# Kernel optimization log

Measured on AMD Instinct MI355X. Metric: run time of the kernel, lower is better.

The kernel has to match this reference:

```python
import jax, jax.numpy as jnp
import numpy as np
from jax import lax

DIM = 256
NUM_HEADS = 8
HEAD_DIM = DIM // NUM_HEADS          # 32
KEY_DIM = int(HEAD_DIM * 0.5)        # 16
SCALE = KEY_DIM ** -0.5
H_QKV = DIM + KEY_DIM * NUM_HEADS * 2  # 512
BN_EPS = 1e-3  # keras BatchNormalization default epsilon


def conv_bn(x, w, gamma, beta, mean, var, groups=1):
    # Conv2D (no bias) + BatchNorm (inference), activation=None
    y = lax.conv_general_dilated(
        x, w, window_strides=(1, 1), padding='SAME',
        dimension_numbers=('NHWC', 'HWIO', 'NHWC'),
        feature_group_count=groups)
    return gamma * (y - mean) * lax.rsqrt(var + BN_EPS) + beta


def setup_inputs() -> dict:
    key = jax.random.key(0)
    ks = jax.random.split(key, 4)
    B, Hs, Ws = 8, 32, 32
    inp = {
        'inputs': jax.random.normal(ks[0], (B, Hs, Ws, DIM), dtype=jnp.float32),
        # qkv: 1x1 conv dim -> h
        'qkv_w': jax.random.normal(ks[1], (1, 1, DIM, H_QKV), dtype=jnp.float32) * 0.05,
        'qkv_gamma': jnp.ones((H_QKV,), jnp.float32),
        'qkv_beta': jnp.zeros((H_QKV,), jnp.float32),
        'qkv_mean': jnp.zeros((H_QKV,), jnp.float32),
        'qkv_var': jnp.ones((H_QKV,), jnp.float32),
        # pe: 3x3 depthwise conv (groups=dim)
        'pe_w': jax.random.normal(ks[2], (3, 3, 1, DIM), dtype=jnp.float32) * 0.05,
        'pe_gamma': jnp.ones((DIM,), jnp.float32),
        'pe_beta': jnp.zeros((DIM,), jnp.float32),
        'pe_mean': jnp.zeros((DIM,), jnp.float32),
        'pe_var': jnp.ones((DIM,), jnp.float32),
        # proj: 1x1 conv dim -> dim
        'proj_w': jax.random.normal(ks[3], (1, 1, DIM, DIM), dtype=jnp.float32) * 0.05,
        'proj_gamma': jnp.ones((DIM,), jnp.float32),
        'proj_beta': jnp.zeros((DIM,), jnp.float32),
        'proj_mean': jnp.zeros((DIM,), jnp.float32),
        'proj_var': jnp.ones((DIM,), jnp.float32),
    }
    return inp


def reference(inputs, qkv_w, qkv_gamma, qkv_beta, qkv_mean, qkv_var,
              pe_w, pe_gamma, pe_beta, pe_mean, pe_var,
              proj_w, proj_gamma, proj_beta, proj_mean, proj_var):
    B, Hs, Ws, C = inputs.shape
    N = Hs * Ws
    x = conv_bn(inputs, qkv_w, qkv_gamma, qkv_beta, qkv_mean, qkv_var)  # [B,H,W,h]
    x = x.reshape(B, N, NUM_HEADS, 2 * KEY_DIM + HEAD_DIM)
    q = x[..., :KEY_DIM]                          # [B,N,nh,kd]
    k = x[..., KEY_DIM:2 * KEY_DIM]               # [B,N,nh,kd]
    v = x[..., 2 * KEY_DIM:]                      # [B,N,nh,hd]
    # attn = q^T @ k^T : [B,nh,N,N]
    attn = jnp.einsum('bnhk,bmhk->bhnm', q, k) * SCALE
    attn = jax.nn.softmax(attn, axis=-1)
    # x = v^T @ attn : [B,nh,hd,N]
    x = jnp.einsum('bnhd,bhnm->bhdm', v, attn)
    # faithful to source: transpose [0,2,1,3] -> [B,hd,nh,N], then reshape NHWC
    x = jnp.transpose(x, (0, 2, 1, 3)).reshape(B, Hs, Ws, C)
    pe = conv_bn(v.reshape(B, Hs, Ws, C), pe_w, pe_gamma, pe_beta, pe_mean, pe_var, groups=C)
    x = x + pe
    x = conv_bn(x, proj_w, proj_gamma, proj_beta, proj_mean, proj_var)
    return x
```

## Files before the change

kernel.cpp:

```cpp
#include <hip/hip_runtime.h>

typedef _Float16 h4 __attribute__((ext_vector_type(4)));
typedef _Float16 h8 __attribute__((ext_vector_type(8)));
typedef float    f4 __attribute__((ext_vector_type(4)));

#define QSCALE (0.25f * 1.44269504088896f)

__device__ __forceinline__ float ex2(float x){ return __builtin_amdgcn_exp2f(x); }

__global__ __launch_bounds__(256) void prep_k(
    const float* __restrict__ qkvw, const float* __restrict__ qg, const float* __restrict__ qb,
    const float* __restrict__ qm,   const float* __restrict__ qv,
    const float* __restrict__ pew,  const float* __restrict__ pg, const float* __restrict__ pb,
    const float* __restrict__ pm,   const float* __restrict__ pv,
    const float* __restrict__ prw,  const float* __restrict__ prg, const float* __restrict__ prb,
    const float* __restrict__ prm,  const float* __restrict__ prv,
    _Float16* __restrict__ Wqkv, float* __restrict__ bqkv,
    _Float16* __restrict__ Wproj, float* __restrict__ bproj,
    float* __restrict__ peW, float* __restrict__ peB)
{
  const int gid = blockIdx.x*256 + threadIdx.x;
  const int gsz = gridDim.x*256;
  for (int i = gid; i < 512*256; i += gsz){
    int o = i >> 8, c = i & 255;
    float s = qg[o] * rsqrtf(qv[o] + 1e-3f);
    Wqkv[i] = (_Float16)(qkvw[c*512 + o] * s);
  }
  for (int i = gid; i < 512; i += gsz){
    float s = qg[i] * rsqrtf(qv[i] + 1e-3f);
    bqkv[i] = qb[i] - qm[i]*s;
  }
  for (int i = gid; i < 256*256; i += gsz){
    int o = i >> 8, c = i & 255;
    float s = prg[o] * rsqrtf(prv[o] + 1e-3f);
    Wproj[i] = (_Float16)(prw[c*256 + o] * s);
  }
  for (int i = gid; i < 256; i += gsz){
    float s = prg[i] * rsqrtf(prv[i] + 1e-3f);
    bproj[i] = prb[i] - prm[i]*s;
  }
  for (int i = gid; i < 9*256; i += gsz){
    int c = i & 255;
    float s = pg[c] * rsqrtf(pv[c] + 1e-3f);
    peW[i] = pew[i] * s;
  }
  for (int i = gid; i < 256; i += gsz){
    float s = pg[i] * rsqrtf(pv[i] + 1e-3f);
    peB[i] = pb[i] - pm[i]*s;
  }
}

__global__ __launch_bounds__(256) void qkv_gemm_k(
    const float* __restrict__ X, const _Float16* __restrict__ Wqkv,
    const float* __restrict__ bias,
    _Float16* __restrict__ Qh, _Float16* __restrict__ Kh, _Float16* __restrict__ Vh)
{
  __shared__ __align__(16) _Float16 As[64*136];
  __shared__ __align__(16) _Float16 Bs[64*136];
  const int t = threadIdx.x, lane = t & 63, wv = t >> 6;
  const int l15 = lane & 15, q = lane >> 4;
  const int wr = wv & 1, wc = wv >> 1;
  const int m0 = blockIdx.x*64, n0 = blockIdx.y*64;
  const int ar = t >> 2, ac = t & 3;
  float4 av[8]; uint4 bv[4];
  #pragma unroll
  for (int i = 0; i < 8; ++i){
    int idx = i*256 + t, row = idx >> 5, c4 = idx & 31;
    av[i] = *(const float4*)(X + (size_t)(m0+row)*256 + c4*4);
  }
  #pragma unroll
  for (int i = 0; i < 4; ++i){
    int idx = i*256 + t, row = idx >> 4, seg = idx & 15;
    bv[i] = *(const uint4*)(Wqkv + (size_t)(n0+row)*256 + seg*8);
  }
  f4 acc[2][2] = {};
  #pragma unroll
  for (int kc = 0; kc < 2; ++kc){
    #pragma unroll
    for (int i = 0; i < 8; ++i){
      int idx = i*256 + t, row = idx >> 5, c4 = idx & 31;
      h4 o; o[0]=(_Float16)av[i].x; o[1]=(_Float16)av[i].y;
            o[2]=(_Float16)av[i].z; o[3]=(_Float16)av[i].w;
      *(h4*)&As[row*136 + c4*4] = o;
    }
    #pragma unroll
    for (int i = 0; i < 4; ++i){
      int idx = i*256 + t, row = idx >> 4, seg = idx & 15;
      *(uint4*)&Bs[row*136 + seg*8] = bv[i];
    }
    __syncthreads();
    if (kc == 0){
      #pragma unroll
      for (int i = 0; i < 8; ++i){
        int idx = i*256 + t, row = idx >> 5, c4 = idx & 31;
        av[i] = *(const float4*)(X + (size_t)(m0+row)*256 + 128 + c4*4);
      }
      #pragma unroll
      for (int i = 0; i < 4; ++i){
        int idx = i*256 + t, row = idx >> 4, seg = idx & 15;
        bv[i] = *(const uint4*)(Wqkv + (size_t)(n0+row)*256 + 128 + seg*8);
      }
    }
    #pragma unroll
    for (int kk = 0; kk < 4; ++kk){
      h8 af[2], bf[2];
      #pragma unroll
      for (int mi = 0; mi < 2; ++mi)
        af[mi] = *(const h8*)&As[(wr*32 + mi*16 + l15)*136 + kk*32 + q*8];
      #pragma unroll
      for (int nj = 0; nj < 2; ++nj)
        bf[nj] = *(const h8*)&Bs[(wc*32 + nj*16 + l15)*136 + kk*32 + q*8];
      #pragma unroll
      for (int mi = 0; mi < 2; ++mi)
      #pragma unroll
      for (int nj = 0; nj < 2; ++nj)
        acc[mi][nj] = __builtin_amdgcn_mfma_f32_16x16x32_f16(af[mi], bf[nj], acc[mi][nj], 0,0,0);
    }
    __syncthreads();
  }
  #pragma unroll
  for (int mi = 0; mi < 2; ++mi)
  #pragma unroll
  for (int nj = 0; nj < 2; ++nj){
    const int og = n0 + wc*32 + nj*16 + l15;
    const int h = og >> 6, j = og & 63;
    const float bs = bias[og];
    #pragma unroll
    for (int r = 0; r < 4; ++r){
      const int mg = m0 + wr*32 + mi*16 + q*4 + r;
      const int b = mg >> 10, n = mg & 1023;
      const size_t bhn = (size_t)(b*8+h)*1024 + n;
      const float v = acc[mi][nj][r] + bs;
      if (j < 16)      Qh[bhn*16 + j]      = (_Float16)(v * QSCALE);
      else if (j < 32) Kh[bhn*16 + (j-16)] = (_Float16)v;
      else             Vh[bhn*32 + (j-32)] = (_Float16)v;
    }
  }
}

__global__ __launch_bounds__(256) void proj_gemm_k(
    const _Float16* __restrict__ A, const _Float16* __restrict__ Wproj,
    const float* __restrict__ bias, float* __restrict__ Out)
{
  __shared__ __align__(16) _Float16 As[64*136];
  __shared__ __align__(16) _Float16 Bs[64*136];
  const int t = threadIdx.x, lane = t & 63, wv = t >> 6;
  const int l15 = lane & 15, q = lane >> 4;
  const int wr = wv & 1, wc = wv >> 1;
  const int m0 = blockIdx.x*64, n0 = blockIdx.y*64;
  uint4 av[4], bv[4];
  #pragma unroll
  for (int i = 0; i < 4; ++i){
    int idx = i*256 + t, row = idx >> 4, seg = idx & 15;
    av[i] = *(const uint4*)(A     + (size_t)(m0+row)*256 + seg*8);
    bv[i] = *(const uint4*)(Wproj + (size_t)(n0+row)*256 + seg*8);
  }
  f4 acc[2][2] = {};
  #pragma unroll
  for (int kc = 0; kc < 2; ++kc){
    #pragma unroll
    for (int i = 0; i < 4; ++i){
      int idx = i*256 + t, row = idx >> 4, seg = idx & 15;
      *(uint4*)&As[row*136 + seg*8] = av[i];
      *(uint4*)&Bs[row*136 + seg*8] = bv[i];
    }
    __syncthreads();
    if (kc == 0){
      #pragma unroll
      for (int i = 0; i < 4; ++i){
        int idx = i*256 + t, row = idx >> 4, seg = idx & 15;
        av[i] = *(const uint4*)(A     + (size_t)(m0+row)*256 + 128 + seg*8);
        bv[i] = *(const uint4*)(Wproj + (size_t)(n0+row)*256 + 128 + seg*8);
      }
    }
    #pragma unroll
    for (int kk = 0; kk < 4; ++kk){
      h8 af[2], bf[2];
      #pragma unroll
      for (int mi = 0; mi < 2; ++mi)
        af[mi] = *(const h8*)&As[(wr*32 + mi*16 + l15)*136 + kk*32 + q*8];
      #pragma unroll
      for (int nj = 0; nj < 2; ++nj)
        bf[nj] = *(const h8*)&Bs[(wc*32 + nj*16 + l15)*136 + kk*32 + q*8];
      #pragma unroll
      for (int mi = 0; mi < 2; ++mi)
      #pragma unroll
      for (int nj = 0; nj < 2; ++nj)
        acc[mi][nj] = __builtin_amdgcn_mfma_f32_16x16x32_f16(af[mi], bf[nj], acc[mi][nj], 0,0,0);
    }
    __syncthreads();
  }
  #pragma unroll
  for (int mi = 0; mi < 2; ++mi)
  #pragma unroll
  for (int nj = 0; nj < 2; ++nj){
    const int og = n0 + wc*32 + nj*16 + l15;
    const float bs = bias[og];
    #pragma unroll
    for (int r = 0; r < 4; ++r){
      const int mg = m0 + wr*32 + mi*16 + q*4 + r;
      Out[(size_t)mg*256 + og] = acc[mi][nj][r] + bs;
    }
  }
}

__global__ __launch_bounds__(256) void pass1_k(
    const _Float16* __restrict__ Qh, const _Float16* __restrict__ Kh,
    const _Float16* __restrict__ Vh, _Float16* __restrict__ Vs)
{
  __shared__ __align__(16) _Float16 Ks[1024*20];
  const int t = threadIdx.x, lane = t & 63, wv = t >> 6;
  const int l15 = lane & 15, q = lane >> 4;
  const int bh = blockIdx.y;
  const int n0 = blockIdx.x*128 + wv*32;
  const size_t qb = (size_t)bh*1024;
  const _Float16* kp = Kh + qb*16;
  #pragma unroll
  for (int i = 0; i < 8; ++i){
    int idx = i*256 + t, row = idx >> 1, seg = idx & 1;
    *(uint4*)&Ks[row*20 + seg*8] = *(const uint4*)(kp + row*16 + seg*8);
  }
  const h4 af0 = *(const h4*)(Qh + (qb + n0 + l15)*16 + q*4);
  const h4 af1 = *(const h4*)(Qh + (qb + n0 + 16 + l15)*16 + q*4);
  __syncthreads();
  f4 sm0 = {0.f,0.f,0.f,0.f}, sm1 = {0.f,0.f,0.f,0.f};
  #pragma unroll 8
  for (int mt = 0; mt < 64; ++mt){
    h4 bf = *(const h4*)&Ks[(mt*16 + l15)*20 + q*4];
    f4 z = {0.f,0.f,0.f,0.f};
    f4 d0 = __builtin_amdgcn_mfma_f32_16x16x16f16(af0, bf, z, 0,0,0);
    f4 d1 = __builtin_amdgcn_mfma_f32_16x16x16f16(af1, bf, z, 0,0,0);
    #pragma unroll
    for (int r = 0; r < 4; ++r){ sm0[r] += ex2(d0[r]); sm1[r] += ex2(d1[r]); }
  }
  #pragma unroll
  for (int st = 1; st < 16; st <<= 1){
    #pragma unroll
    for (int r = 0; r < 4; ++r){
      sm0[r] += __shfl_xor(sm0[r], st, 64);
      sm1[r] += __shfl_xor(sm1[r], st, 64);
    }
  }
  f4 cv0, cv1;
  #pragma unroll
  for (int r = 0; r < 4; ++r){ cv0[r] = 1.0f/sm0[r]; cv1[r] = 1.0f/sm1[r]; }
  #pragma unroll
  for (int half = 0; half < 2; ++half){
    const int dd = l15 + half*16;
    h4 o0, o1;
    #pragma unroll
    for (int r = 0; r < 4; ++r){
      o0[r] = (_Float16)((float)Vh[(qb + n0 + q*4 + r)*32 + dd] * cv0[r]);
      o1[r] = (_Float16)((float)Vh[(qb + n0 + 16 + q*4 + r)*32 + dd] * cv1[r]);
    }
    *(h4*)(Vs + ((size_t)bh*32 + dd)*1024 + n0 + q*4)      = o0;
    *(h4*)(Vs + ((size_t)bh*32 + dd)*1024 + n0 + 16 + q*4) = o1;
  }
}

__global__ __launch_bounds__(256) void pass2_k(
    const _Float16* __restrict__ Qh, const _Float16* __restrict__ Kh,
    const _Float16* __restrict__ Vs, _Float16* __restrict__ X1h)
{
  __shared__ __align__(16) char smem[1024*20*2 + 32*264*2];
  _Float16* Qs  = (_Float16*)smem;
  _Float16* Vss = (_Float16*)(smem + 40960);
  float*    Tt  = (float*)smem;
  const int t = threadIdx.x, lane = t & 63, wv = t >> 6;
  const int l15 = lane & 15, q = lane >> 4;
  const int bh = blockIdx.y;
  const int b  = bh >> 3, h = bh & 7;
  const int mb = blockIdx.x*128 + wv*32;
  const size_t qb = (size_t)bh*1024;
  const h4 kf0 = *(const h4*)(Kh + (qb + mb + l15)*16 + q*4);
  const h4 kf1 = *(const h4*)(Kh + (qb + mb + 16 + l15)*16 + q*4);
  const _Float16* qp = Qh + qb*16;
  const _Float16* vp = Vs + (size_t)bh*32*1024;
  #pragma unroll
  for (int i = 0; i < 8; ++i){
    int idx = i*256 + t, row = idx >> 1, seg = idx & 1;
    *(uint4*)&Qs[row*20 + seg*8] = *(const uint4*)(qp + row*16 + seg*8);
  }
  uint4 vr[4];
  #pragma unroll
  for (int i = 0; i < 4; ++i){
    int idx = i*256 + t, d = idx >> 5, seg = idx & 31;
    vr[i] = *(const uint4*)(vp + (size_t)d*1024 + seg*8);
  }
  f4 a00={0.f,0.f,0.f,0.f}, a01={0.f,0.f,0.f,0.f};
  f4 a10={0.f,0.f,0.f,0.f}, a11={0.f,0.f,0.f,0.f};
  for (int c = 0; c < 4; ++c){
    const int nt = c*256;
    #pragma unroll
    for (int i = 0; i < 4; ++i){
      int idx = i*256 + t, d = idx >> 5, seg = idx & 31;
      *(uint4*)&Vss[d*264 + seg*8] = vr[i];
    }
    __syncthreads();
    if (c < 3){
      #pragma unroll
      for (int i = 0; i < 4; ++i){
        int idx = i*256 + t, d = idx >> 5, seg = idx & 31;
        vr[i] = *(const uint4*)(vp + (size_t)d*1024 + nt + 256 + seg*8);
      }
    }
    #pragma unroll 4
    for (int sub = 0; sub < 16; ++sub){
      h4 qf = *(const h4*)&Qs[(nt + sub*16 + l15)*20 + q*4];
      h4 b0 = *(const h4*)&Vss[l15*264      + sub*16 + q*4];
      h4 b1 = *(const h4*)&Vss[(16+l15)*264 + sub*16 + q*4];
      f4 z = {0.f,0.f,0.f,0.f};
      f4 s0 = __builtin_amdgcn_mfma_f32_16x16x16f16(qf, kf0, z, 0,0,0);
      f4 s1 = __builtin_amdgcn_mfma_f32_16x16x16f16(qf, kf1, z, 0,0,0);
      h4 p0, p1;
      #pragma unroll
      for (int r = 0; r < 4; ++r){ p0[r] = (_Float16)ex2(s0[r]); p1[r] = (_Float16)ex2(s1[r]); }
      a00 = __builtin_amdgcn_mfma_f32_16x16x16f16(p0, b0, a00, 0,0,0);
      a01 = __builtin_amdgcn_mfma_f32_16x16x16f16(p0, b1, a01, 0,0,0);
      a10 = __builtin_amdgcn_mfma_f32_16x16x16f16(p1, b0, a10, 0,0,0);
      a11 = __builtin_amdgcn_mfma_f32_16x16x16f16(p1, b1, a11, 0,0,0);
    }
    __syncthreads();
  }
  float* tw = Tt + wv*(32*33);
  #pragma unroll
  for (int r = 0; r < 4; ++r){
    tw[(q*4 + r)*33      + l15]      = a00[r];
    tw[(q*4 + r)*33      + 16 + l15] = a01[r];
    tw[(16 + q*4 + r)*33 + l15]      = a10[r];
    tw[(16 + q*4 + r)*33 + 16 + l15] = a11[r];
  }
  __syncthreads();
  _Float16* xb = X1h + (size_t)b*262144 + (size_t)h*1024 + mb;
  const int mloc = lane & 31, dh = lane >> 5;
  #pragma unroll
  for (int r = 0; r < 16; ++r){
    const int d = r*2 + dh;
    xb[(size_t)d*8192 + mloc] = (_Float16)tw[mloc*33 + d];
  }
}

__global__ __launch_bounds__(256) void pe_add_k(
    const _Float16* __restrict__ Vh, const _Float16* __restrict__ X1h,
    const float* __restrict__ peW, const float* __restrict__ peB,
    _Float16* __restrict__ X2h)
{
  const int u = blockIdx.x*256 + threadIdx.x;
  const int c0 = (u & 31) * 8;
  const int tok = u >> 5;
  const int b = tok >> 10, n = tok & 1023;
  const int hs = n >> 5, ws = n & 31;
  const int h = c0 >> 5, d0 = c0 & 31;
  const size_t idx8 = (size_t)tok*256 + c0;
  float acc[8];
  {
    f4 b0v = *(const f4*)(peB + c0), b1v = *(const f4*)(peB + c0 + 4);
    #pragma unroll
    for (int j = 0; j < 4; ++j){ acc[j] = b0v[j]; acc[4+j] = b1v[j]; }
  }
  const _Float16* vb = Vh + (size_t)(b*8 + h)*32768 + d0;
  #pragma unroll
  for (int dy = 0; dy < 3; ++dy){
    const int y = hs + dy - 1;
    if ((unsigned)y < 32u){
      #pragma unroll
      for (int dx = 0; dx < 3; ++dx){
        const int x = ws + dx - 1;
        if ((unsigned)x < 32u){
          const int kk = dy*3 + dx;
          h8 vv = *(const h8*)(vb + (size_t)(y*32 + x)*32);
          f4 w0 = *(const f4*)(peW + kk*256 + c0);
          f4 w1 = *(const f4*)(peW + kk*256 + c0 + 4);
          #pragma unroll
          for (int j = 0; j < 4; ++j){
            acc[j]   += w0[j] * (float)vv[j];
            acc[4+j] += w1[j] * (float)vv[4+j];
          }
        }
      }
    }
  }
  h8 x1 = *(const h8*)(X1h + idx8);
  h8 o;
  #pragma unroll
  for (int j = 0; j < 8; ++j) o[j] = (_Float16)((float)x1[j] + acc[j]);
  *(h8*)(X2h + idx8) = o;
}

extern "C" void kernel_launch(void* const* d_in, const int* in_sizes, int n_in,
                              void* d_out, int out_size, void* d_ws, size_t ws_size,
                              hipStream_t stream)
{
  const float* X    = (const float*)d_in[0];
  const float* qkvw = (const float*)d_in[1];
  const float* qg   = (const float*)d_in[2];
  const float* qb   = (const float*)d_in[3];
  const float* qm   = (const float*)d_in[4];
  const float* qv   = (const float*)d_in[5];
  const float* pew  = (const float*)d_in[6];
  const float* pg   = (const float*)d_in[7];
  const float* pb   = (const float*)d_in[8];
  const float* pm   = (const float*)d_in[9];
  const float* pv   = (const float*)d_in[10];
  const float* prw  = (const float*)d_in[11];
  const float* prg  = (const float*)d_in[12];
  const float* prb  = (const float*)d_in[13];
  const float* prm  = (const float*)d_in[14];
  const float* prv  = (const float*)d_in[15];

  char* ws = (char*)d_ws;
  _Float16* X2h   = (_Float16*)(ws + 0);
  _Float16* Qh    = (_Float16*)(ws + 4194304);
  _Float16* Kh    = (_Float16*)(ws + 6291456);
  _Float16* Vh    = (_Float16*)(ws + 8388608);
  _Float16* Vs    = (_Float16*)(ws + 12582912);
  _Float16* X1h   = (_Float16*)(ws + 16777216);
  _Float16* Wqkv  = (_Float16*)(ws + 20971520);
  float*    bqkv  = (float*)   (ws + 21233664);
  _Float16* Wproj = (_Float16*)(ws + 21235712);
  float*    bproj = (float*)   (ws + 21366784);
  float*    peW   = (float*)   (ws + 21367808);
  float*    peB   = (float*)   (ws + 21377024);

  prep_k<<<64, 256, 0, stream>>>(qkvw, qg, qb, qm, qv, pew, pg, pb, pm, pv,
                                 prw, prg, prb, prm, prv,
                                 Wqkv, bqkv, Wproj, bproj, peW, peB);
  qkv_gemm_k<<<dim3(128, 8), 256, 0, stream>>>(X, Wqkv, bqkv, Qh, Kh, Vh);
  pass1_k<<<dim3(8, 64), 256, 0, stream>>>(Qh, Kh, Vh, Vs);
  pass2_k<<<dim3(8, 64), 256, 0, stream>>>(Qh, Kh, Vs, X1h);
  pe_add_k<<<1024, 256, 0, stream>>>(Vh, X1h, peW, peB, X2h);
  proj_gemm_k<<<dim3(128, 4), 256, 0, stream>>>(X2h, Wproj, bproj, (float*)d_out);
}
```

Before: 185.7 us.

## Stream K/Q/V through small LDS tiles in attention passes to raise occupancy

Pass1 and pass2 used to load the whole 1024-row K (or Q) plus a 256-column V chunk into shared memory per block, about 40-57KB of LDS. They now stream 128-row chunks with register double-buffering, cutting LDS to about 6-17KB so more blocks can be resident per CU. The grid is also transposed so consecutive block IDs step through different batch-heads. The cost is eight barrier pairs per block instead of one or four, and less work between each sync.

```diff
diff --git a/kernel.cpp b/kernel.cpp
--- a/kernel.cpp
+++ b/kernel.cpp
@@ -61,7 +61,6 @@
   const int l15 = lane & 15, q = lane >> 4;
   const int wr = wv & 1, wc = wv >> 1;
   const int m0 = blockIdx.x*64, n0 = blockIdx.y*64;
-  const int ar = t >> 2, ac = t & 3;
   float4 av[8]; uint4 bv[4];
   #pragma unroll
   for (int i = 0; i < 8; ++i){
@@ -208,30 +207,32 @@
     const _Float16* __restrict__ Qh, const _Float16* __restrict__ Kh,
     const _Float16* __restrict__ Vh, _Float16* __restrict__ Vs)
 {
-  __shared__ __align__(16) _Float16 Ks[1024*20];
+  __shared__ __align__(16) _Float16 Ks[128*24];
   const int t = threadIdx.x, lane = t & 63, wv = t >> 6;
   const int l15 = lane & 15, q = lane >> 4;
-  const int bh = blockIdx.y;
-  const int n0 = blockIdx.x*128 + wv*32;
+  const int bh = blockIdx.x;
+  const int n0 = blockIdx.y*128 + wv*32;
   const size_t qb = (size_t)bh*1024;
-  const _Float16* kp = Kh + qb*16;
-  #pragma unroll
-  for (int i = 0; i < 8; ++i){
-    int idx = i*256 + t, row = idx >> 1, seg = idx & 1;
-    *(uint4*)&Ks[row*20 + seg*8] = *(const uint4*)(kp + row*16 + seg*8);
-  }
   const h4 af0 = *(const h4*)(Qh + (qb + n0 + l15)*16 + q*4);
   const h4 af1 = *(const h4*)(Qh + (qb + n0 + 16 + l15)*16 + q*4);
-  __syncthreads();
+  const _Float16* kp = Kh + qb*16;
+  const int row = t >> 1, seg = t & 1;
+  uint4 kr = *(const uint4*)(kp + row*16 + seg*8);
   f4 sm0 = {0.f,0.f,0.f,0.f}, sm1 = {0.f,0.f,0.f,0.f};
-  #pragma unroll 8
-  for (int mt = 0; mt < 64; ++mt){
-    h4 bf = *(const h4*)&Ks[(mt*16 + l15)*20 + q*4];
-    f4 z = {0.f,0.f,0.f,0.f};
-    f4 d0 = __builtin_amdgcn_mfma_f32_16x16x16f16(af0, bf, z, 0,0,0);
-    f4 d1 = __builtin_amdgcn_mfma_f32_16x16x16f16(af1, bf, z, 0,0,0);
-    #pragma unroll
-    for (int r = 0; r < 4; ++r){ sm0[r] += ex2(d0[r]); sm1[r] += ex2(d1[r]); }
+  for (int c = 0; c < 8; ++c){
+    *(uint4*)&Ks[row*24 + seg*8] = kr;
+    __syncthreads();
+    if (c < 7) kr = *(const uint4*)(kp + ((c+1)*128 + row)*16 + seg*8);
+    #pragma unroll
+    for (int sub = 0; sub < 8; ++sub){
+      h4 bf = *(const h4*)&Ks[(sub*16 + l15)*24 + q*4];
+      f4 z = {0.f,0.f,0.f,0.f};
+      f4 d0 = __builtin_amdgcn_mfma_f32_16x16x16f16(af0, bf, z, 0,0,0);
+      f4 d1 = __builtin_amdgcn_mfma_f32_16x16x16f16(af1, bf, z, 0,0,0);
+      #pragma unroll
+      for (int r = 0; r < 4; ++r){ sm0[r] += ex2(d0[r]); sm1[r] += ex2(d1[r]); }
+    }
+    __syncthreads();
   }
   #pragma unroll
   for (int st = 1; st < 16; st <<= 1){
@@ -262,53 +263,43 @@
     const _Float16* __restrict__ Qh, const _Float16* __restrict__ Kh,
     const _Float16* __restrict__ Vs, _Float16* __restrict__ X1h)
 {
-  __shared__ __align__(16) char smem[1024*20*2 + 32*264*2];
+  __shared__ __align__(16) char smem[16896];
   _Float16* Qs  = (_Float16*)smem;
-  _Float16* Vss = (_Float16*)(smem + 40960);
+  _Float16* Vss = (_Float16*)(smem + 6144);
   float*    Tt  = (float*)smem;
   const int t = threadIdx.x, lane = t & 63, wv = t >> 6;
   const int l15 = lane & 15, q = lane >> 4;
-  const int bh = blockIdx.y;
+  const int bh = blockIdx.x;
   const int b  = bh >> 3, h = bh & 7;
-  const int mb = blockIdx.x*128 + wv*32;
+  const int mb = blockIdx.y*128 + wv*32;
   const size_t qb = (size_t)bh*1024;
   const h4 kf0 = *(const h4*)(Kh + (qb + mb + l15)*16 + q*4);
   const h4 kf1 = *(const h4*)(Kh + (qb + mb + 16 + l15)*16 + q*4);
   const _Float16* qp = Qh + qb*16;
   const _Float16* vp = Vs + (size_t)bh*32*1024;
-  #pragma unroll
-  for (int i = 0; i < 8; ++i){
-    int idx = i*256 + t, row = idx >> 1, seg = idx & 1;
-    *(uint4*)&Qs[row*20 + seg*8] = *(const uint4*)(qp + row*16 + seg*8);
-  }
-  uint4 vr[4];
-  #pragma unroll
-  for (int i = 0; i < 4; ++i){
-    int idx = i*256 + t, d = idx >> 5, seg = idx & 31;
-    vr[i] = *(const uint4*)(vp + (size_t)d*1024 + seg*8);
-  }
+  const int row = t >> 1, seg = t & 1;
+  const int vd = t >> 4, vseg = t & 15;
+  uint4 qr = *(const uint4*)(qp + row*16 + seg*8);
+  uint4 vr0 = *(const uint4*)(vp + (size_t)vd*1024      + vseg*8);
+  uint4 vr1 = *(const uint4*)(vp + (size_t)(vd+16)*1024 + vseg*8);
   f4 a00={0.f,0.f,0.f,0.f}, a01={0.f,0.f,0.f,0.f};
   f4 a10={0.f,0.f,0.f,0.f}, a11={0.f,0.f,0.f,0.f};
-  for (int c = 0; c < 4; ++c){
-    const int nt = c*256;
-    #pragma unroll
-    for (int i = 0; i < 4; ++i){
-      int idx = i*256 + t, d = idx >> 5, seg = idx & 31;
-      *(uint4*)&Vss[d*264 + seg*8] = vr[i];
-    }
-    __syncthreads();
-    if (c < 3){
-      #pragma unroll
-      for (int i = 0; i < 4; ++i){
-        int idx = i*256 + t, d = idx >> 5, seg = idx & 31;
-        vr[i] = *(const uint4*)(vp + (size_t)d*1024 + nt + 256 + seg*8);
-      }
-    }
-    #pragma unroll 4
-    for (int sub = 0; sub < 16; ++sub){
-      h4 qf = *(const h4*)&Qs[(nt + sub*16 + l15)*20 + q*4];
-      h4 b0 = *(const h4*)&Vss[l15*264      + sub*16 + q*4];
-      h4 b1 = *(const h4*)&Vss[(16+l15)*264 + sub*16 + q*4];
+  for (int c = 0; c < 8; ++c){
+    *(uint4*)&Qs[row*24 + seg*8] = qr;
+    *(uint4*)&Vss[vd*136      + vseg*8] = vr0;
+    *(uint4*)&Vss[(vd+16)*136 + vseg*8] = vr1;
+    __syncthreads();
+    if (c < 7){
+      const int nn = (c+1)*128;
+      qr  = *(const uint4*)(qp + (nn + row)*16 + seg*8);
+      vr0 = *(const uint4*)(vp + (size_t)vd*1024      + nn + vseg*8);
+      vr1 = *(const uint4*)(vp + (size_t)(vd+16)*1024 + nn + vseg*8);
+    }
+    #pragma unroll
+    for (int sub = 0; sub < 8; ++sub){
+      h4 qf = *(const h4*)&Qs[(sub*16 + l15)*24 + q*4];
+      h4 b0 = *(const h4*)&Vss[l15*136      + sub*16 + q*4];
+      h4 b1 = *(const h4*)&Vss[(16+l15)*136 + sub*16 + q*4];
       f4 z = {0.f,0.f,0.f,0.f};
       f4 s0 = __builtin_amdgcn_mfma_f32_16x16x16f16(qf, kf0, z, 0,0,0);
       f4 s1 = __builtin_amdgcn_mfma_f32_16x16x16f16(qf, kf1, z, 0,0,0);
@@ -426,8 +417,8 @@
                                  prw, prg, prb, prm, prv,
                                  Wqkv, bqkv, Wproj, bproj, peW, peB);
   qkv_gemm_k<<<dim3(128, 8), 256, 0, stream>>>(X, Wqkv, bqkv, Qh, Kh, Vh);
-  pass1_k<<<dim3(8, 64), 256, 0, stream>>>(Qh, Kh, Vh, Vs);
-  pass2_k<<<dim3(8, 64), 256, 0, stream>>>(Qh, Kh, Vs, X1h);
+  pass1_k<<<dim3(64, 8), 256, 0, stream>>>(Qh, Kh, Vh, Vs);
+  pass2_k<<<dim3(64, 8), 256, 0, stream>>>(Qh, Kh, Vs, X1h);
   pe_add_k<<<1024, 256, 0, stream>>>(Vh, X1h, peW, peB, X2h);
   proj_gemm_k<<<dim3(128, 4), 256, 0, stream>>>(X2h, Wproj, bproj, (float*)d_out);
 }
```

Result: faster. 159.1 us (-14.4%).

## Split attention passes along the key dimension across wave pairs to double block count

Applied to the files above, without the earlier changes.

Both attention passes now give each block 64 query/key rows instead of 128 and split the 1024-long reduction dimension between two wave pairs. Partial softmax sums and partial PV accumulators are combined through shared memory. K and Q/V tiles are streamed in 128-row chunks with register prefetch rather than staged whole, which shrinks LDS use. The goal is twice as many blocks (1024 per pass on 256 CUs) and higher occupancy, at the cost of extra syncs and a shared-memory reduction.

```diff
diff --git a/kernel.cpp b/kernel.cpp
--- a/kernel.cpp
+++ b/kernel.cpp
@@ -61,7 +61,6 @@
   const int l15 = lane & 15, q = lane >> 4;
   const int wr = wv & 1, wc = wv >> 1;
   const int m0 = blockIdx.x*64, n0 = blockIdx.y*64;
-  const int ar = t >> 2, ac = t & 3;
   float4 av[8]; uint4 bv[4];
   #pragma unroll
   for (int i = 0; i < 8; ++i){
@@ -208,30 +207,49 @@
     const _Float16* __restrict__ Qh, const _Float16* __restrict__ Kh,
     const _Float16* __restrict__ Vh, _Float16* __restrict__ Vs)
 {
-  __shared__ __align__(16) _Float16 Ks[1024*20];
+  __shared__ __align__(16) _Float16 Ks[2][128*24];
+  __shared__ float red[2][2][32];
   const int t = threadIdx.x, lane = t & 63, wv = t >> 6;
   const int l15 = lane & 15, q = lane >> 4;
+  const int g = wv & 1, mh = wv >> 1;
   const int bh = blockIdx.y;
-  const int n0 = blockIdx.x*128 + wv*32;
+  const int n0 = blockIdx.x*64 + g*32;
   const size_t qb = (size_t)bh*1024;
-  const _Float16* kp = Kh + qb*16;
-  #pragma unroll
-  for (int i = 0; i < 8; ++i){
-    int idx = i*256 + t, row = idx >> 1, seg = idx & 1;
-    *(uint4*)&Ks[row*20 + seg*8] = *(const uint4*)(kp + row*16 + seg*8);
-  }
   const h4 af0 = *(const h4*)(Qh + (qb + n0 + l15)*16 + q*4);
   const h4 af1 = *(const h4*)(Qh + (qb + n0 + 16 + l15)*16 + q*4);
-  __syncthreads();
+  const _Float16* kp = Kh + qb*16;
+  const int tidp = g*64 + lane;
+  uint4 kr[2];
+  #pragma unroll
+  for (int i = 0; i < 2; ++i){
+    int idx = i*128 + tidp, row = idx >> 1, seg = idx & 1;
+    kr[i] = *(const uint4*)(kp + (mh*512 + row)*16 + seg*8);
+  }
   f4 sm0 = {0.f,0.f,0.f,0.f}, sm1 = {0.f,0.f,0.f,0.f};
-  #pragma unroll 8
-  for (int mt = 0; mt < 64; ++mt){
-    h4 bf = *(const h4*)&Ks[(mt*16 + l15)*20 + q*4];
-    f4 z = {0.f,0.f,0.f,0.f};
-    f4 d0 = __builtin_amdgcn_mfma_f32_16x16x16f16(af0, bf, z, 0,0,0);
-    f4 d1 = __builtin_amdgcn_mfma_f32_16x16x16f16(af1, bf, z, 0,0,0);
-    #pragma unroll
-    for (int r = 0; r < 4; ++r){ sm0[r] += ex2(d0[r]); sm1[r] += ex2(d1[r]); }
+  for (int c = 0; c < 4; ++c){
+    #pragma unroll
+    for (int i = 0; i < 2; ++i){
+      int idx = i*128 + tidp, row = idx >> 1, seg = idx & 1;
+      *(uint4*)&Ks[mh][row*24 + seg*8] = kr[i];
+    }
+    __syncthreads();
+    if (c < 3){
+      #pragma unroll
+      for (int i = 0; i < 2; ++i){
+        int idx = i*128 + tidp, row = idx >> 1, seg = idx & 1;
+        kr[i] = *(const uint4*)(kp + (mh*512 + (c+1)*128 + row)*16 + seg*8);
+      }
+    }
+    #pragma unroll
+    for (int sub = 0; sub < 8; ++sub){
+      h4 bf = *(const h4*)&Ks[mh][(sub*16 + l15)*24 + q*4];
+      f4 z = {0.f,0.f,0.f,0.f};
+      f4 d0 = __builtin_amdgcn_mfma_f32_16x16x16f16(af0, bf, z, 0,0,0);
+      f4 d1 = __builtin_amdgcn_mfma_f32_16x16x16f16(af1, bf, z, 0,0,0);
+      #pragma unroll
+      for (int r = 0; r < 4; ++r){ sm0[r] += ex2(d0[r]); sm1[r] += ex2(d1[r]); }
+    }
+    __syncthreads();
   }
   #pragma unroll
   for (int st = 1; st < 16; st <<= 1){
@@ -241,74 +259,93 @@
       sm1[r] += __shfl_xor(sm1[r], st, 64);
     }
   }
-  f4 cv0, cv1;
-  #pragma unroll
-  for (int r = 0; r < 4; ++r){ cv0[r] = 1.0f/sm0[r]; cv1[r] = 1.0f/sm1[r]; }
-  #pragma unroll
-  for (int half = 0; half < 2; ++half){
-    const int dd = l15 + half*16;
-    h4 o0, o1;
-    #pragma unroll
-    for (int r = 0; r < 4; ++r){
-      o0[r] = (_Float16)((float)Vh[(qb + n0 + q*4 + r)*32 + dd] * cv0[r]);
-      o1[r] = (_Float16)((float)Vh[(qb + n0 + 16 + q*4 + r)*32 + dd] * cv1[r]);
-    }
-    *(h4*)(Vs + ((size_t)bh*32 + dd)*1024 + n0 + q*4)      = o0;
-    *(h4*)(Vs + ((size_t)bh*32 + dd)*1024 + n0 + 16 + q*4) = o1;
-  }
+  if (l15 == 0){
+    #pragma unroll
+    for (int r = 0; r < 4; ++r){
+      red[g][mh][q*4 + r]      = sm0[r];
+      red[g][mh][16 + q*4 + r] = sm1[r];
+    }
+  }
+  __syncthreads();
+  const int dd = l15 + mh*16;
+  h4 o0, o1;
+  #pragma unroll
+  for (int r = 0; r < 4; ++r){
+    const float cv0 = 1.0f/(red[g][0][q*4 + r]      + red[g][1][q*4 + r]);
+    const float cv1 = 1.0f/(red[g][0][16 + q*4 + r] + red[g][1][16 + q*4 + r]);
+    o0[r] = (_Float16)((float)Vh[(qb + n0 + q*4 + r)*32 + dd] * cv0);
+    o1[r] = (_Float16)((float)Vh[(qb + n0 + 16 + q*4 + r)*32 + dd] * cv1);
+  }
+  *(h4*)(Vs + ((size_t)bh*32 + dd)*1024 + n0 + q*4)      = o0;
+  *(h4*)(Vs + ((size_t)bh*32 + dd)*1024 + n0 + 16 + q*4) = o1;
 }
 
 __global__ __launch_bounds__(256) void pass2_k(
     const _Float16* __restrict__ Qh, const _Float16* __restrict__ Kh,
     const _Float16* __restrict__ Vs, _Float16* __restrict__ X1h)
 {
-  __shared__ __align__(16) char smem[1024*20*2 + 32*264*2];
-  _Float16* Qs  = (_Float16*)smem;
-  _Float16* Vss = (_Float16*)(smem + 40960);
-  float*    Tt  = (float*)smem;
+  __shared__ __align__(16) char smem[27648];
+  _Float16* QsB  = (_Float16*)smem;
+  _Float16* VssB = (_Float16*)(smem + 10240);
+  float*    Tt   = (float*)smem;
   const int t = threadIdx.x, lane = t & 63, wv = t >> 6;
   const int l15 = lane & 15, q = lane >> 4;
+  const int mt = wv & 1, nh = wv >> 1;
   const int bh = blockIdx.y;
   const int b  = bh >> 3, h = bh & 7;
-  const int mb = blockIdx.x*128 + wv*32;
+  const int mbase = blockIdx.x*64;
+  const int mb = mbase + mt*32;
   const size_t qb = (size_t)bh*1024;
   const h4 kf0 = *(const h4*)(Kh + (qb + mb + l15)*16 + q*4);
   const h4 kf1 = *(const h4*)(Kh + (qb + mb + 16 + l15)*16 + q*4);
   const _Float16* qp = Qh + qb*16;
   const _Float16* vp = Vs + (size_t)bh*32*1024;
-  #pragma unroll
-  for (int i = 0; i < 8; ++i){
-    int idx = i*256 + t, row = idx >> 1, seg = idx & 1;
-    *(uint4*)&Qs[row*20 + seg*8] = *(const uint4*)(qp + row*16 + seg*8);
-  }
-  uint4 vr[4];
+  _Float16* Qs  = QsB  + nh*(128*20);
+  _Float16* Vss = VssB + nh*(32*136);
+  const int tidp = mt*64 + lane;
+  uint4 qr[2], vr[4];
+  #pragma unroll
+  for (int i = 0; i < 2; ++i){
+    int idx = i*128 + tidp, row = idx >> 1, seg = idx & 1;
+    qr[i] = *(const uint4*)(qp + (nh*512 + row)*16 + seg*8);
+  }
   #pragma unroll
   for (int i = 0; i < 4; ++i){
-    int idx = i*256 + t, d = idx >> 5, seg = idx & 31;
-    vr[i] = *(const uint4*)(vp + (size_t)d*1024 + seg*8);
+    int idx = i*128 + tidp, d = idx >> 4, nseg = idx & 15;
+    vr[i] = *(const uint4*)(vp + (size_t)d*1024 + nh*512 + nseg*8);
   }
   f4 a00={0.f,0.f,0.f,0.f}, a01={0.f,0.f,0.f,0.f};
   f4 a10={0.f,0.f,0.f,0.f}, a11={0.f,0.f,0.f,0.f};
   for (int c = 0; c < 4; ++c){
-    const int nt = c*256;
+    #pragma unroll
+    for (int i = 0; i < 2; ++i){
+      int idx = i*128 + tidp, row = idx >> 1, seg = idx & 1;
+      *(uint4*)&Qs[row*20 + seg*8] = qr[i];
+    }
     #pragma unroll
     for (int i = 0; i < 4; ++i){
-      int idx = i*256 + t, d = idx >> 5, seg = idx & 31;
-      *(uint4*)&Vss[d*264 + seg*8] = vr[i];
+      int idx = i*128 + tidp, d = idx >> 4, nseg = idx & 15;
+      *(uint4*)&Vss[d*136 + nseg*8] = vr[i];
     }
     __syncthreads();
     if (c < 3){
+      const int nn = nh*512 + (c+1)*128;
+      #pragma unroll
+      for (int i = 0; i < 2; ++i){
+        int idx = i*128 + tidp, row = idx >> 1, seg = idx & 1;
+        qr[i] = *(const uint4*)(qp + (nn + row)*16 + seg*8);
+      }
       #pragma unroll
       for (int i = 0; i < 4; ++i){
-        int idx = i*256 + t, d = idx >> 5, seg = idx & 31;
-        vr[i] = *(const uint4*)(vp + (size_t)d*1024 + nt + 256 + seg*8);
-      }
-    }
-    #pragma unroll 4
-    for (int sub = 0; sub < 16; ++sub){
-      h4 qf = *(const h4*)&Qs[(nt + sub*16 + l15)*20 + q*4];
-      h4 b0 = *(const h4*)&Vss[l15*264      + sub*16 + q*4];
-      h4 b1 = *(const h4*)&Vss[(16+l15)*264 + sub*16 + q*4];
+        int idx = i*128 + tidp, d = idx >> 4, nseg = idx & 15;
+        vr[i] = *(const uint4*)(vp + (size_t)d*1024 + nn + nseg*8);
+      }
+    }
+    #pragma unroll
+    for (int sub = 0; sub < 8; ++sub){
+      h4 qf = *(const h4*)&Qs[(sub*16 + l15)*20 + q*4];
+      h4 b0 = *(const h4*)&Vss[l15*136      + sub*16 + q*4];
+      h4 b1 = *(const h4*)&Vss[(16+l15)*136 + sub*16 + q*4];
       f4 z = {0.f,0.f,0.f,0.f};
       f4 s0 = __builtin_amdgcn_mfma_f32_16x16x16f16(qf, kf0, z, 0,0,0);
       f4 s1 = __builtin_amdgcn_mfma_f32_16x16x16f16(qf, kf1, z, 0,0,0);
@@ -322,19 +359,32 @@
     }
     __syncthreads();
   }
-  float* tw = Tt + wv*(32*33);
-  #pragma unroll
-  for (int r = 0; r < 4; ++r){
-    tw[(q*4 + r)*33      + l15]      = a00[r];
-    tw[(q*4 + r)*33      + 16 + l15] = a01[r];
-    tw[(16 + q*4 + r)*33 + l15]      = a10[r];
-    tw[(16 + q*4 + r)*33 + 16 + l15] = a11[r];
+  float* tw = Tt + mt*(32*33);
+  if (nh == 0){
+    #pragma unroll
+    for (int r = 0; r < 4; ++r){
+      tw[(q*4 + r)*33      + l15]      = a00[r];
+      tw[(q*4 + r)*33      + 16 + l15] = a01[r];
+      tw[(16 + q*4 + r)*33 + l15]      = a10[r];
+      tw[(16 + q*4 + r)*33 + 16 + l15] = a11[r];
+    }
+  }
+  __syncthreads();
+  if (nh == 1){
+    #pragma unroll
+    for (int r = 0; r < 4; ++r){
+      tw[(q*4 + r)*33      + l15]      += a00[r];
+      tw[(q*4 + r)*33      + 16 + l15] += a01[r];
+      tw[(16 + q*4 + r)*33 + l15]      += a10[r];
+      tw[(16 + q*4 + r)*33 + 16 + l15] += a11[r];
+    }
   }
   __syncthreads();
   _Float16* xb = X1h + (size_t)b*262144 + (size_t)h*1024 + mb;
   const int mloc = lane & 31, dh = lane >> 5;
   #pragma unroll
-  for (int r = 0; r < 16; ++r){
+  for (int i = 0; i < 8; ++i){
+    const int r = nh*8 + i;
     const int d = r*2 + dh;
     xb[(size_t)d*8192 + mloc] = (_Float16)tw[mloc*33 + d];
   }
@@ -426,8 +476,8 @@
                                  prw, prg, prb, prm, prv,
                                  Wqkv, bqkv, Wproj, bproj, peW, peB);
   qkv_gemm_k<<<dim3(128, 8), 256, 0, stream>>>(X, Wqkv, bqkv, Qh, Kh, Vh);
-  pass1_k<<<dim3(8, 64), 256, 0, stream>>>(Qh, Kh, Vh, Vs);
-  pass2_k<<<dim3(8, 64), 256, 0, stream>>>(Qh, Kh, Vs, X1h);
+  pass1_k<<<dim3(16, 64), 256, 0, stream>>>(Qh, Kh, Vh, Vs);
+  pass2_k<<<dim3(16, 64), 256, 0, stream>>>(Qh, Kh, Vs, X1h);
   pe_add_k<<<1024, 256, 0, stream>>>(Vh, X1h, peW, peB, X2h);
   proj_gemm_k<<<dim3(128, 4), 256, 0, stream>>>(X2h, Wproj, bproj, (float*)d_out);
 }
```

Measured after the change: 185.9 us. About the same (+0.1%).
